# Kernel optimization log

Hardware: AMD Instinct MI355X
Metric: run time of the kernel (lower is better)

The kernel has to match this reference:

```python
import jax, jax.numpy as jnp
import numpy as np

B, S, D_IN, D_H = 2048, 256, 128, 256
C2 = 2.7193  # time-decay log offset from the original module


def setup_inputs() -> dict:
    key = jax.random.key(0)
    k0, k1, k2, k3 = jax.random.split(key, 4)
    inputs = jax.random.normal(k0, (B, S, D_IN), dtype=jnp.float32)
    # time must be increasing so intervals are positive (log(dt + 2.7193) valid)
    dt = jax.random.uniform(k1, (B, S), minval=0.1, maxval=5.0, dtype=jnp.float32)
    time = jnp.cumsum(dt, axis=1)
    Wi = jax.random.normal(k2, (D_IN, D_H), dtype=jnp.float32) / np.sqrt(D_IN).astype(np.float32)
    bi = jnp.zeros((D_H,), dtype=jnp.float32)
    Wh = jax.random.normal(k3, (D_H, D_H), dtype=jnp.float32) / np.sqrt(D_H).astype(np.float32)
    bh = jnp.zeros((D_H,), dtype=jnp.float32)
    return {"inputs": inputs, "time": time, "Wi": Wi, "bi": bi, "Wh": Wh, "bh": bh}


def reference(inputs, time, Wi, bi, Wh, bh):
    Bsz, Slen, _ = inputs.shape
    H = Wh.shape[0]
    # time points -> intervals, then decay weight 1/log(dt + c2)
    dt = time[:, 1:] - time[:, :-1]                     # [B, S-1]
    w = 1.0 / jnp.log(dt + C2)                          # [B, S-1]
    # precompute all input projections once (original recomputes per gate)
    x_proj = jnp.einsum('bsd,dh->bsh', inputs[:, :-1], Wi) + bi  # [B, S-1, H]

    def step(carry, xs):
        h, c, o = carry
        xz, wt = xs                                     # xz:[B,H], wt:[B]
        z = xz + h @ Wh + bh                            # shared gate pre-activation
        g = jax.nn.sigmoid(z)                           # f_t == i_t == o_t (same linears in source)
        C_bar = jnp.tanh(z)
        C_S = jnp.tanh(c @ Wh + bh)                     # short-term memory
        C_star = (c - C_S) + C_S * wt[:, None]          # long-term + discounted short-term
        c_new = g * C_star + g * C_bar
        h_new = g * jnp.tanh(C_bar)
        return (h_new, c_new, g), None

    zeros = jnp.zeros((Bsz, H), dtype=inputs.dtype)
    (h, c, o), _ = jax.lax.scan(
        step, (zeros, zeros, zeros),
        (jnp.swapaxes(x_proj, 0, 1), w.T),
    )
    res = o @ Wh + bh                                   # linear_hidden(o_t) of last step
    return jnp.stack((res, h, c))                       # [3, B, H]
```

## Files before the change

### kernel.cpp

```cpp
#include <hip/hip_runtime.h>

typedef __attribute__((ext_vector_type(8))) short short8;
typedef __attribute__((ext_vector_type(4))) float floatx4;
typedef __attribute__((ext_vector_type(2))) float floatx2;
typedef __attribute__((ext_vector_type(2))) unsigned uintx2;

#define LOG2E 1.44269504088896340736f

#define BAR() asm volatile("s_waitcnt lgkmcnt(0)\n\ts_barrier" ::: "memory")

__device__ __forceinline__ floatx2 F2(float v) { return (floatx2){v, v}; }

__device__ __forceinline__ unsigned short f2bf(float f) {
  unsigned u = __float_as_uint(f);
  u += 0x7FFFu + ((u >> 16) & 1u);
  return (unsigned short)(u >> 16);
}

__device__ __forceinline__ unsigned cvtpk(float lo, float hi) {
  unsigned r;
  asm("v_cvt_pk_bf16_f32 %0, %1, %2" : "=v"(r) : "v"(lo), "v"(hi));
  return r;
}

__global__ __launch_bounds__(512, 1) void tlstm_kernel(
    const float* __restrict__ x, const float* __restrict__ tim,
    const float* __restrict__ Wi, const float* __restrict__ bi,
    const float* __restrict__ Wh, const float* __restrict__ bh,
    float* __restrict__ out)
{
  __shared__ __align__(16) unsigned short Sst[2 * 4224];
  __shared__ __align__(16) unsigned short Sx[2 * 2176];
  __shared__ __align__(16) float WMt[2048];

  const int tid = threadIdx.x;
  const int wv  = tid >> 6;
  const int l   = tid & 63;
  const int q   = l >> 4;
  const int r   = l & 15;
  const int b0  = blockIdx.x * 8;

  const int col1 = wv * 32 + r;
  const int col2 = col1 + 16;

  short8 wh[2][8];
#pragma unroll
  for (int tx = 0; tx < 2; ++tx)
#pragma unroll
    for (int c = 0; c < 8; ++c)
#pragma unroll
      for (int j = 0; j < 8; ++j)
        wh[tx][c][j] = (short)f2bf(Wh[(c * 32 + q * 8 + j) * 256 + wv * 32 + tx * 16 + r]);
  short8 wi[2][4];
#pragma unroll
  for (int tx = 0; tx < 2; ++tx)
#pragma unroll
    for (int c = 0; c < 4; ++c)
#pragma unroll
      for (int j = 0; j < 8; ++j)
        wi[tx][c][j] = (short)f2bf(Wi[(c * 32 + q * 8 + j) * 256 + wv * 32 + tx * 16 + r]);
  const float bh1 = bh[col1], bh2 = bh[col2];
  const float bi1 = bi[col1], bi2 = bi[col2];

  const int raS = r * 264 + q * 8;
  const int raX = r * 136 + q * 8;
  const int wrA = (4 * q) * 264 + col1;
  const int xw  = (2 * wv + (l >> 5)) * 136 + 4 * (l & 31);
  const float* xbase = x + (long)(b0 + wv) * 32768 + (l >> 5) * 128 + 4 * (l & 31);

  {
    unsigned* S32 = (unsigned*)Sst;
    for (int i = tid; i < 2112; i += 512) S32[i] = 0;
  }
  for (int i = tid; i < 2040; i += 512) {
    int t = i >> 3, bl = i & 7;
    float t0 = tim[(b0 + bl) * 256 + t];
    float t1 = tim[(b0 + bl) * 256 + t + 1];
    WMt[i] = 1.f - 1.f / logf(t1 - t0 + 2.7193f);
  }
  {
    floatx4 v = *(const floatx4*)xbase;
    uintx2 pk = {cvtpk(v.x, v.y), cvtpk(v.z, v.w)};
    *(uintx2*)&Sx[xw] = pk;
  }
  __syncthreads();

  floatx2 cP0 = F2(0.f), cP1 = F2(0.f);
  floatx2 hP0 = F2(0.f), hP1 = F2(0.f);
  floatx2 gP0 = F2(0.f), gP1 = F2(0.f);
  int xro = 0;

  auto proc2 = [&](floatx2 zin, floatx2 cpin, floatx2& cio, floatx2& gio,
                   floatx2& hio, float wmv, int ih0, int ih1, int woff) {
    floatx2 z  = __builtin_elementwise_min(__builtin_elementwise_max(zin,  F2(-10.f)), F2(10.f));
    floatx2 cp = __builtin_elementwise_min(__builtin_elementwise_max(cpin, F2(-10.f)), F2(10.f));
    floatx2 mz = z * F2(-LOG2E);
    floatx2 u  = {__builtin_amdgcn_exp2f(mz.x), __builtin_amdgcn_exp2f(mz.y)};
    floatx2 u2 = u * u;
    floatx2 mc = cp * F2(-2.f * LOG2E);
    floatx2 v  = {__builtin_amdgcn_exp2f(mc.x), __builtin_amdgcn_exp2f(mc.y)};
    floatx2 a1 = u + F2(1.f), a2 = u2 + F2(1.f), a3 = v + F2(1.f);
    floatx2 p12 = a1 * a2;
    floatx2 pr  = p12 * a3;
    floatx2 D   = {__builtin_amdgcn_rcpf(pr.x), __builtin_amdgcn_rcpf(pr.y)};
    floatx2 Da3 = D * a3;
    floatx2 g   = Da3 * a2;
    floatx2 ir2 = Da3 * a1;
    floatx2 ir3 = D * p12;
    floatx2 Cb  = ir2 - u2 * ir2;
    floatx2 Cs  = ir3 - v * ir3;
    floatx2 Cst = cio - Cs * F2(wmv);
    floatx2 cn  = g * (Cst + Cb);
    floatx2 s   = Cb * Cb;
    floatx2 P   = F2(0.003592028f);
    P = P * s + F2(-0.008863236f);
    P = P * s + F2(0.021869488f);
    P = P * s + F2(-0.053968254f);
    P = P * s + F2(0.133333333f);
    P = P * s + F2(-0.333333333f);
    P = P * s + F2(1.0f);
    floatx2 hn = g * (Cb * P);
    unsigned pk0 = cvtpk(hn.x, cn.x);
    unsigned pk1 = cvtpk(hn.y, cn.y);
    Sst[woff + ih0]       = (unsigned short)pk0;
    Sst[woff + ih0 + 264] = (unsigned short)(pk0 >> 16);
    Sst[woff + ih1]       = (unsigned short)pk1;
    Sst[woff + ih1 + 264] = (unsigned short)(pk1 >> 16);
    cio = cn; gio = g; hio = hn;
  };

  floatx4 xa1, xa2;
  auto loadx = [&]() {
    short8 xf[4];
#pragma unroll
    for (int c = 0; c < 4; ++c)
      xf[c] = *(const short8*)&Sx[xro + raX + 32 * c];
    floatx4 x1 = {bi1, bi1, bi1, bi1};
    floatx4 x2 = {bi2, bi2, bi2, bi2};
#pragma unroll
    for (int c = 0; c < 4; ++c) {
      x1 = __builtin_amdgcn_mfma_f32_16x16x32_bf16(xf[c], wi[0][c], x1, 0, 0, 0);
      x2 = __builtin_amdgcn_mfma_f32_16x16x32_bf16(xf[c], wi[1][c], x2, 0, 0, 0);
    }
    xa1 = x1; xa2 = x2;
  };

  auto dostep = [&](int roff, int woff, int par, int wmoff) {
    short8 sf[8];
#pragma unroll
    for (int c = 0; c < 8; ++c)
      sf[c] = *(const short8*)&Sst[roff + raS + 32 * c];
    floatx4 a1e = {bh1, bh1, bh1, bh1}, a1o = {0.f, 0.f, 0.f, 0.f};
    floatx4 a2e = {bh2, bh2, bh2, bh2}, a2o = {0.f, 0.f, 0.f, 0.f};
#pragma unroll
    for (int c = 0; c < 8; c += 2) {
      a1e = __builtin_amdgcn_mfma_f32_16x16x32_bf16(sf[c],     wh[0][c],     a1e, 0, 0, 0);
      a1o = __builtin_amdgcn_mfma_f32_16x16x32_bf16(sf[c + 1], wh[0][c + 1], a1o, 0, 0, 0);
      a2e = __builtin_amdgcn_mfma_f32_16x16x32_bf16(sf[c],     wh[1][c],     a2e, 0, 0, 0);
      a2o = __builtin_amdgcn_mfma_f32_16x16x32_bf16(sf[c + 1], wh[1][c + 1], a2o, 0, 0, 0);
    }
    floatx4 A1 = a1e + a1o;
    floatx4 A2 = a2e + a2o;
    floatx2 wm = *(const floatx2*)&WMt[wmoff];
    floatx2 z0  = {A1[0] + xa1[par],     A2[0] + xa2[par]};
    floatx2 cp0 = {A1[1],                A2[1]};
    floatx2 z1  = {A1[2] + xa1[2 + par], A2[2] + xa2[2 + par]};
    floatx2 cp1 = {A1[3],                A2[3]};
    proc2(z0, cp0, cP0, gP0, hP0, wm.x, wrA,       wrA + 16,  woff);
    proc2(z1, cp1, cP1, gP1, hP1, wm.y, wrA + 528, wrA + 544, woff);
    BAR();
  };

  for (int p = 0; p < 127; ++p) {
    floatx4 nv = *(const floatx4*)(xbase + (p + 1) * 256);
    loadx();
    dostep(0, 4224, 0, 16 * p + 2 * q);
    {
      uintx2 pk = {cvtpk(nv.x, nv.y), cvtpk(nv.z, nv.w)};
      *(uintx2*)&Sx[(xro ^ 2176) + xw] = pk;
    }
    dostep(4224, 0, 1, 16 * p + 8 + 2 * q);
    xro ^= 2176;
  }

  loadx();
  dostep(0, 4224, 0, 16 * 127 + 2 * q);

  Sst[wrA]       = f2bf(gP0.x);  Sst[wrA + 264] = 0;
  Sst[wrA + 528] = f2bf(gP1.x);  Sst[wrA + 792] = 0;
  Sst[wrA + 16]  = f2bf(gP0.y);  Sst[wrA + 280] = 0;
  Sst[wrA + 544] = f2bf(gP1.y);  Sst[wrA + 808] = 0;
  BAR();
  short8 gf[8];
#pragma unroll
  for (int c = 0; c < 8; ++c)
    gf[c] = *(const short8*)&Sst[raS + 32 * c];
  floatx4 r1 = {bh1, bh1, bh1, bh1};
  floatx4 r2 = {bh2, bh2, bh2, bh2};
#pragma unroll
  for (int c = 0; c < 8; ++c) {
    r1 = __builtin_amdgcn_mfma_f32_16x16x32_bf16(gf[c], wh[0][c], r1, 0, 0, 0);
    r2 = __builtin_amdgcn_mfma_f32_16x16x32_bf16(gf[c], wh[1][c], r2, 0, 0, 0);
  }

  const long P  = 2048L * 256;
  const long o0 = (long)(b0 + 2 * q) * 256;
  const long o1 = (long)(b0 + 2 * q + 1) * 256;
  out[o0 + col1]         = r1[0];
  out[o1 + col1]         = r1[2];
  out[o0 + col2]         = r2[0];
  out[o1 + col2]         = r2[2];
  out[P + o0 + col1]     = hP0.x;
  out[P + o1 + col1]     = hP1.x;
  out[P + o0 + col2]     = hP0.y;
  out[P + o1 + col2]     = hP1.y;
  out[2 * P + o0 + col1] = cP0.x;
  out[2 * P + o1 + col1] = cP1.x;
  out[2 * P + o0 + col2] = cP0.y;
  out[2 * P + o1 + col2] = cP1.y;
}

extern "C" void kernel_launch(void* const* d_in, const int* in_sizes, int n_in,
                              void* d_out, int out_size, void* d_ws, size_t ws_size,
                              hipStream_t stream) {
  const float* xin = (const float*)d_in[0];
  const float* tim = (const float*)d_in[1];
  const float* Wi  = (const float*)d_in[2];
  const float* bi  = (const float*)d_in[3];
  const float* Wh  = (const float*)d_in[4];
  const float* bh  = (const float*)d_in[5];
  tlstm_kernel<<<dim3(256), dim3(512), 0, stream>>>(xin, tim, Wi, bi, Wh, bh, (float*)d_out);
}
```

Baseline: 254.3 us.

## Halve batch rows per block and launch twice as many blocks

Each block now handles 4 batch rows instead of 8, giving 512 blocks and allowing 2 blocks per CU via launch bounds. Each thread keeps one column pair of state instead of two, which cuts the elementwise gate work per step and halves the shared-memory footprint. The aim is to spread the serial recurrence over all CUs and overlap two blocks' latency chains per CU. In exchange, the MFMA tiles are half-filled (rows 8-15 read duplicated data), so matrix work per useful row doubles, and register pressure must fit in the 2-block limit.

Measured after the change: 347.6 us. +36.7%, slower.

```diff
diff --git a/kernel.cpp b/kernel.cpp
--- a/kernel.cpp
+++ b/kernel.cpp
@@ -3,7 +3,6 @@
 typedef __attribute__((ext_vector_type(8))) short short8;
 typedef __attribute__((ext_vector_type(4))) float floatx4;
 typedef __attribute__((ext_vector_type(2))) float floatx2;
-typedef __attribute__((ext_vector_type(2))) unsigned uintx2;
 
 #define LOG2E 1.44269504088896340736f
 
@@ -23,25 +22,29 @@
   return r;
 }
 
-__global__ __launch_bounds__(512, 1) void tlstm_kernel(
+__global__ __launch_bounds__(512, 2) void tlstm_kernel(
     const float* __restrict__ x, const float* __restrict__ tim,
     const float* __restrict__ Wi, const float* __restrict__ bi,
     const float* __restrict__ Wh, const float* __restrict__ bh,
     float* __restrict__ out)
 {
-  __shared__ __align__(16) unsigned short Sst[2 * 4224];
-  __shared__ __align__(16) unsigned short Sx[2 * 2176];
-  __shared__ __align__(16) float WMt[2048];
+  __shared__ __align__(16) unsigned short Sst[2 * 2112];
+  __shared__ __align__(16) unsigned short Sx[2 * 1088];
+  __shared__ __align__(16) float WMt[1020];
 
   const int tid = threadIdx.x;
   const int wv  = tid >> 6;
   const int l   = tid & 63;
   const int q   = l >> 4;
   const int r   = l & 15;
-  const int b0  = blockIdx.x * 8;
+  const int r8  = r & 7;
+  const int q1  = q & 1;
+  const int qt  = q >> 1;
+  const int b0  = blockIdx.x * 4;
 
   const int col1 = wv * 32 + r;
   const int col2 = col1 + 16;
+  const int wcol = wv * 32 + qt * 16 + r;
 
   short8 wh[2][8];
 #pragma unroll
@@ -62,36 +65,32 @@
   const float bh1 = bh[col1], bh2 = bh[col2];
   const float bi1 = bi[col1], bi2 = bi[col2];
 
-  const int raS = r * 264 + q * 8;
-  const int raX = r * 136 + q * 8;
-  const int wrA = (4 * q) * 264 + col1;
-  const int xw  = (2 * wv + (l >> 5)) * 136 + 4 * (l & 31);
-  const float* xbase = x + (long)(b0 + wv) * 32768 + (l >> 5) * 128 + 4 * (l & 31);
+  const int raS = r8 * 264 + q * 8;
+  const int raX = r8 * 136 + q * 8;
+  const int ih0 = (4 * q1) * 264 + wcol;
+  const int xw  = wv * 136 + 2 * l;
+  const float* xbase = x + (long)(b0 + (wv >> 1)) * 32768 + (wv & 1) * 128 + 2 * l;
 
   {
     unsigned* S32 = (unsigned*)Sst;
-    for (int i = tid; i < 2112; i += 512) S32[i] = 0;
-  }
-  for (int i = tid; i < 2040; i += 512) {
-    int t = i >> 3, bl = i & 7;
+    for (int i = tid; i < 1056; i += 512) S32[i] = 0;
+  }
+  for (int i = tid; i < 1020; i += 512) {
+    int t = i >> 2, bl = i & 3;
     float t0 = tim[(b0 + bl) * 256 + t];
     float t1 = tim[(b0 + bl) * 256 + t + 1];
     WMt[i] = 1.f - 1.f / logf(t1 - t0 + 2.7193f);
   }
   {
-    floatx4 v = *(const floatx4*)xbase;
-    uintx2 pk = {cvtpk(v.x, v.y), cvtpk(v.z, v.w)};
-    *(uintx2*)&Sx[xw] = pk;
+    floatx2 v = *(const floatx2*)xbase;
+    *(unsigned*)&Sx[xw] = cvtpk(v.x, v.y);
   }
   __syncthreads();
 
-  floatx2 cP0 = F2(0.f), cP1 = F2(0.f);
-  floatx2 hP0 = F2(0.f), hP1 = F2(0.f);
-  floatx2 gP0 = F2(0.f), gP1 = F2(0.f);
+  floatx2 cS = F2(0.f), hS = F2(0.f), gS = F2(0.f);
   int xro = 0;
 
-  auto proc2 = [&](floatx2 zin, floatx2 cpin, floatx2& cio, floatx2& gio,
-                   floatx2& hio, float wmv, int ih0, int ih1, int woff) {
+  auto proc2 = [&](floatx2 zin, floatx2 cpin, floatx2 wmv, int woff) {
     floatx2 z  = __builtin_elementwise_min(__builtin_elementwise_max(zin,  F2(-10.f)), F2(10.f));
     floatx2 cp = __builtin_elementwise_min(__builtin_elementwise_max(cpin, F2(-10.f)), F2(10.f));
     floatx2 mz = z * F2(-LOG2E);
@@ -109,7 +108,7 @@
     floatx2 ir3 = D * p12;
     floatx2 Cb  = ir2 - u2 * ir2;
     floatx2 Cs  = ir3 - v * ir3;
-    floatx2 Cst = cio - Cs * F2(wmv);
+    floatx2 Cst = cS - Cs * wmv;
     floatx2 cn  = g * (Cst + Cb);
     floatx2 s   = Cb * Cb;
     floatx2 P   = F2(0.003592028f);
@@ -124,12 +123,12 @@
     unsigned pk1 = cvtpk(hn.y, cn.y);
     Sst[woff + ih0]       = (unsigned short)pk0;
     Sst[woff + ih0 + 264] = (unsigned short)(pk0 >> 16);
-    Sst[woff + ih1]       = (unsigned short)pk1;
-    Sst[woff + ih1 + 264] = (unsigned short)(pk1 >> 16);
-    cio = cn; gio = g; hio = hn;
+    Sst[woff + ih0 + 528] = (unsigned short)pk1;
+    Sst[woff + ih0 + 792] = (unsigned short)(pk1 >> 16);
+    cS = cn; gS = g; hS = hn;
   };
 
-  floatx4 xa1, xa2;
+  floatx4 xs;
   auto loadx = [&]() {
     short8 xf[4];
 #pragma unroll
@@ -142,7 +141,7 @@
       x1 = __builtin_amdgcn_mfma_f32_16x16x32_bf16(xf[c], wi[0][c], x1, 0, 0, 0);
       x2 = __builtin_amdgcn_mfma_f32_16x16x32_bf16(xf[c], wi[1][c], x2, 0, 0, 0);
     }
-    xa1 = x1; xa2 = x2;
+    xs = qt ? x2 : x1;
   };
 
   auto dostep = [&](int roff, int woff, int par, int wmoff) {
@@ -150,46 +149,35 @@
 #pragma unroll
     for (int c = 0; c < 8; ++c)
       sf[c] = *(const short8*)&Sst[roff + raS + 32 * c];
-    floatx4 a1e = {bh1, bh1, bh1, bh1}, a1o = {0.f, 0.f, 0.f, 0.f};
-    floatx4 a2e = {bh2, bh2, bh2, bh2}, a2o = {0.f, 0.f, 0.f, 0.f};
-#pragma unroll
-    for (int c = 0; c < 8; c += 2) {
-      a1e = __builtin_amdgcn_mfma_f32_16x16x32_bf16(sf[c],     wh[0][c],     a1e, 0, 0, 0);
-      a1o = __builtin_amdgcn_mfma_f32_16x16x32_bf16(sf[c + 1], wh[0][c + 1], a1o, 0, 0, 0);
-      a2e = __builtin_amdgcn_mfma_f32_16x16x32_bf16(sf[c],     wh[1][c],     a2e, 0, 0, 0);
-      a2o = __builtin_amdgcn_mfma_f32_16x16x32_bf16(sf[c + 1], wh[1][c + 1], a2o, 0, 0, 0);
+    floatx4 a1 = {bh1, bh1, bh1, bh1};
+    floatx4 a2 = {bh2, bh2, bh2, bh2};
+#pragma unroll
+    for (int c = 0; c < 8; ++c) {
+      a1 = __builtin_amdgcn_mfma_f32_16x16x32_bf16(sf[c], wh[0][c], a1, 0, 0, 0);
+      a2 = __builtin_amdgcn_mfma_f32_16x16x32_bf16(sf[c], wh[1][c], a2, 0, 0, 0);
     }
-    floatx4 A1 = a1e + a1o;
-    floatx4 A2 = a2e + a2o;
-    floatx2 wm = *(const floatx2*)&WMt[wmoff];
-    floatx2 z0  = {A1[0] + xa1[par],     A2[0] + xa2[par]};
-    floatx2 cp0 = {A1[1],                A2[1]};
-    floatx2 z1  = {A1[2] + xa1[2 + par], A2[2] + xa2[2 + par]};
-    floatx2 cp1 = {A1[3],                A2[3]};
-    proc2(z0, cp0, cP0, gP0, hP0, wm.x, wrA,       wrA + 16,  woff);
-    proc2(z1, cp1, cP1, gP1, hP1, wm.y, wrA + 528, wrA + 544, woff);
+    floatx4 As = qt ? a2 : a1;
+    floatx2 wm = *(const floatx2*)&WMt[wmoff + 2 * q1];
+    floatx2 z  = {As[0] + xs[par], As[2] + xs[2 + par]};
+    floatx2 cp = {As[1],           As[3]};
+    proc2(z, cp, wm, woff);
     BAR();
   };
 
   for (int p = 0; p < 127; ++p) {
-    floatx4 nv = *(const floatx4*)(xbase + (p + 1) * 256);
+    floatx2 nv = *(const floatx2*)(xbase + (p + 1) * 256);
     loadx();
-    dostep(0, 4224, 0, 16 * p + 2 * q);
-    {
-      uintx2 pk = {cvtpk(nv.x, nv.y), cvtpk(nv.z, nv.w)};
-      *(uintx2*)&Sx[(xro ^ 2176) + xw] = pk;
-    }
-    dostep(4224, 0, 1, 16 * p + 8 + 2 * q);
-    xro ^= 2176;
+    dostep(0, 2112, 0, 8 * p);
+    *(unsigned*)&Sx[(xro ^ 1088) + xw] = cvtpk(nv.x, nv.y);
+    dostep(2112, 0, 1, 8 * p + 4);
+    xro ^= 1088;
   }
 
   loadx();
-  dostep(0, 4224, 0, 16 * 127 + 2 * q);
-
-  Sst[wrA]       = f2bf(gP0.x);  Sst[wrA + 264] = 0;
-  Sst[wrA + 528] = f2bf(gP1.x);  Sst[wrA + 792] = 0;
-  Sst[wrA + 16]  = f2bf(gP0.y);  Sst[wrA + 280] = 0;
-  Sst[wrA + 544] = f2bf(gP1.y);  Sst[wrA + 808] = 0;
+  dostep(0, 2112, 0, 8 * 127);
+
+  Sst[ih0]       = f2bf(gS.x);  Sst[ih0 + 264] = 0;
+  Sst[ih0 + 528] = f2bf(gS.y);  Sst[ih0 + 792] = 0;
   BAR();
   short8 gf[8];
 #pragma unroll
@@ -202,22 +190,17 @@
     r1 = __builtin_amdgcn_mfma_f32_16x16x32_bf16(gf[c], wh[0][c], r1, 0, 0, 0);
     r2 = __builtin_amdgcn_mfma_f32_16x16x32_bf16(gf[c], wh[1][c], r2, 0, 0, 0);
   }
+  floatx4 rs = qt ? r2 : r1;
 
   const long P  = 2048L * 256;
-  const long o0 = (long)(b0 + 2 * q) * 256;
-  const long o1 = (long)(b0 + 2 * q + 1) * 256;
-  out[o0 + col1]         = r1[0];
-  out[o1 + col1]         = r1[2];
-  out[o0 + col2]         = r2[0];
-  out[o1 + col2]         = r2[2];
-  out[P + o0 + col1]     = hP0.x;
-  out[P + o1 + col1]     = hP1.x;
-  out[P + o0 + col2]     = hP0.y;
-  out[P + o1 + col2]     = hP1.y;
-  out[2 * P + o0 + col1] = cP0.x;
-  out[2 * P + o1 + col1] = cP1.x;
-  out[2 * P + o0 + col2] = cP0.y;
-  out[2 * P + o1 + col2] = cP1.y;
+  const long o0 = (long)(b0 + 2 * q1) * 256;
+  const long o1 = o0 + 256;
+  out[o0 + wcol]         = rs[0];
+  out[o1 + wcol]         = rs[2];
+  out[P + o0 + wcol]     = hS.x;
+  out[P + o1 + wcol]     = hS.y;
+  out[2 * P + o0 + wcol] = cS.x;
+  out[2 * P + o1 + wcol] = cS.y;
 }
 
 extern "C" void kernel_launch(void* const* d_in, const int* in_sizes, int n_in,
@@ -229,5 +212,5 @@
   const float* bi  = (const float*)d_in[3];
   const float* Wh  = (const float*)d_in[4];
   const float* bh  = (const float*)d_in[5];
-  tlstm_kernel<<<dim3(256), dim3(512), 0, stream>>>(xin, tim, Wi, bi, Wh, bh, (float*)d_out);
-}
+  tlstm_kernel<<<dim3(512), dim3(512), 0, stream>>>(xin, tim, Wi, bi, Wh, bh, (float*)d_out);
+}
```

## Fold -log2e into weights and prefetch x projection one step ahead

Applied to the files above, without the earlier changes.

Scales Wh, Wi and both biases by -log2(e) at load time so the exp2 arguments come straight from the MFMA accumulators, which removes per-element multiplies. The final linear output is rescaled by -ln2 to undo this. The input projection for the next step pair is now computed one step early, and global x loads are prefetched two steps ahead with the first two slices staged up front, so the x MFMAs sit off the serial recurrence path. The split even/odd accumulators are replaced by single serial MFMA chains, and the lane-to-row mapping in proc2 is rearranged. Risks include extra bf16 rounding error from the scaled weights, higher register pressure, and longer MFMA dependency chains.

Measured after the change: 270.2 us. 6.2% more time.

```diff
diff --git a/kernel.cpp b/kernel.cpp
--- a/kernel.cpp
+++ b/kernel.cpp
@@ -5,7 +5,9 @@
 typedef __attribute__((ext_vector_type(2))) float floatx2;
 typedef __attribute__((ext_vector_type(2))) unsigned uintx2;
 
-#define LOG2E 1.44269504088896340736f
+#define NLOG2E -1.44269504088896340736f
+#define NLN2   -0.69314718055994530942f
+#define CLMP    14.4269504089f
 
 #define BAR() asm volatile("s_waitcnt lgkmcnt(0)\n\ts_barrier" ::: "memory")
 
@@ -50,7 +52,7 @@
     for (int c = 0; c < 8; ++c)
 #pragma unroll
       for (int j = 0; j < 8; ++j)
-        wh[tx][c][j] = (short)f2bf(Wh[(c * 32 + q * 8 + j) * 256 + wv * 32 + tx * 16 + r]);
+        wh[tx][c][j] = (short)f2bf(NLOG2E * Wh[(c * 32 + q * 8 + j) * 256 + wv * 32 + tx * 16 + r]);
   short8 wi[2][4];
 #pragma unroll
   for (int tx = 0; tx < 2; ++tx)
@@ -58,14 +60,14 @@
     for (int c = 0; c < 4; ++c)
 #pragma unroll
       for (int j = 0; j < 8; ++j)
-        wi[tx][c][j] = (short)f2bf(Wi[(c * 32 + q * 8 + j) * 256 + wv * 32 + tx * 16 + r]);
-  const float bh1 = bh[col1], bh2 = bh[col2];
-  const float bi1 = bi[col1], bi2 = bi[col2];
-
-  const int raS = r * 264 + q * 8;
-  const int raX = r * 136 + q * 8;
-  const int wrA = (4 * q) * 264 + col1;
-  const int xw  = (2 * wv + (l >> 5)) * 136 + 4 * (l & 31);
+        wi[tx][c][j] = (short)f2bf(NLOG2E * Wi[(c * 32 + q * 8 + j) * 256 + wv * 32 + tx * 16 + r]);
+  const float bh1 = NLOG2E * bh[col1], bh2 = NLOG2E * bh[col2];
+  const float bi1 = NLOG2E * bi[col1], bi2 = NLOG2E * bi[col2];
+
+  const int raS  = r * 264 + q * 8;
+  const int raX  = r * 136 + q * 8;
+  const int ihT1 = (4 * q) * 264 + col1;
+  const int xw   = (2 * wv + (l >> 5)) * 136 + 4 * (l & 31);
   const float* xbase = x + (long)(b0 + wv) * 32768 + (l >> 5) * 128 + 4 * (l & 31);
 
   {
@@ -79,26 +81,28 @@
     WMt[i] = 1.f - 1.f / logf(t1 - t0 + 2.7193f);
   }
   {
-    floatx4 v = *(const floatx4*)xbase;
-    uintx2 pk = {cvtpk(v.x, v.y), cvtpk(v.z, v.w)};
-    *(uintx2*)&Sx[xw] = pk;
+    floatx4 v0 = *(const floatx4*)xbase;
+    uintx2 p0 = {cvtpk(v0.x, v0.y), cvtpk(v0.z, v0.w)};
+    *(uintx2*)&Sx[xw] = p0;
+    floatx4 v1 = *(const floatx4*)(xbase + 256);
+    uintx2 p1 = {cvtpk(v1.x, v1.y), cvtpk(v1.z, v1.w)};
+    *(uintx2*)&Sx[2176 + xw] = p1;
   }
   __syncthreads();
 
-  floatx2 cP0 = F2(0.f), cP1 = F2(0.f);
-  floatx2 hP0 = F2(0.f), hP1 = F2(0.f);
-  floatx2 gP0 = F2(0.f), gP1 = F2(0.f);
+  floatx2 cT1 = F2(0.f), cT2 = F2(0.f);
+  floatx2 hT1 = F2(0.f), hT2 = F2(0.f);
+  floatx2 gT1 = F2(0.f), gT2 = F2(0.f);
   int xro = 0;
 
   auto proc2 = [&](floatx2 zin, floatx2 cpin, floatx2& cio, floatx2& gio,
-                   floatx2& hio, float wmv, int ih0, int ih1, int woff) {
-    floatx2 z  = __builtin_elementwise_min(__builtin_elementwise_max(zin,  F2(-10.f)), F2(10.f));
-    floatx2 cp = __builtin_elementwise_min(__builtin_elementwise_max(cpin, F2(-10.f)), F2(10.f));
-    floatx2 mz = z * F2(-LOG2E);
-    floatx2 u  = {__builtin_amdgcn_exp2f(mz.x), __builtin_amdgcn_exp2f(mz.y)};
+                   floatx2& hio, floatx2 wm, int ih, int woff) {
+    floatx2 z  = __builtin_elementwise_min(__builtin_elementwise_max(zin,  F2(-CLMP)), F2(CLMP));
+    floatx2 cp = __builtin_elementwise_min(__builtin_elementwise_max(cpin, F2(-CLMP)), F2(CLMP));
+    floatx2 u  = {__builtin_amdgcn_exp2f(z.x), __builtin_amdgcn_exp2f(z.y)};
     floatx2 u2 = u * u;
-    floatx2 mc = cp * F2(-2.f * LOG2E);
-    floatx2 v  = {__builtin_amdgcn_exp2f(mc.x), __builtin_amdgcn_exp2f(mc.y)};
+    floatx2 c2 = cp + cp;
+    floatx2 v  = {__builtin_amdgcn_exp2f(c2.x), __builtin_amdgcn_exp2f(c2.y)};
     floatx2 a1 = u + F2(1.f), a2 = u2 + F2(1.f), a3 = v + F2(1.f);
     floatx2 p12 = a1 * a2;
     floatx2 pr  = p12 * a3;
@@ -109,7 +113,7 @@
     floatx2 ir3 = D * p12;
     floatx2 Cb  = ir2 - u2 * ir2;
     floatx2 Cs  = ir3 - v * ir3;
-    floatx2 Cst = cio - Cs * F2(wmv);
+    floatx2 Cst = cio - Cs * wm;
     floatx2 cn  = g * (Cst + Cb);
     floatx2 s   = Cb * Cb;
     floatx2 P   = F2(0.003592028f);
@@ -122,19 +126,18 @@
     floatx2 hn = g * (Cb * P);
     unsigned pk0 = cvtpk(hn.x, cn.x);
     unsigned pk1 = cvtpk(hn.y, cn.y);
-    Sst[woff + ih0]       = (unsigned short)pk0;
-    Sst[woff + ih0 + 264] = (unsigned short)(pk0 >> 16);
-    Sst[woff + ih1]       = (unsigned short)pk1;
-    Sst[woff + ih1 + 264] = (unsigned short)(pk1 >> 16);
+    Sst[woff + ih]       = (unsigned short)pk0;
+    Sst[woff + ih + 264] = (unsigned short)(pk0 >> 16);
+    Sst[woff + ih + 528] = (unsigned short)pk1;
+    Sst[woff + ih + 792] = (unsigned short)(pk1 >> 16);
     cio = cn; gio = g; hio = hn;
   };
 
-  floatx4 xa1, xa2;
-  auto loadx = [&]() {
+  auto loadx = [&](int xoff, floatx4& x1o, floatx4& x2o) {
     short8 xf[4];
 #pragma unroll
     for (int c = 0; c < 4; ++c)
-      xf[c] = *(const short8*)&Sx[xro + raX + 32 * c];
+      xf[c] = *(const short8*)&Sx[xoff + raX + 32 * c];
     floatx4 x1 = {bi1, bi1, bi1, bi1};
     floatx4 x2 = {bi2, bi2, bi2, bi2};
 #pragma unroll
@@ -142,54 +145,54 @@
       x1 = __builtin_amdgcn_mfma_f32_16x16x32_bf16(xf[c], wi[0][c], x1, 0, 0, 0);
       x2 = __builtin_amdgcn_mfma_f32_16x16x32_bf16(xf[c], wi[1][c], x2, 0, 0, 0);
     }
-    xa1 = x1; xa2 = x2;
+    x1o = x1; x2o = x2;
   };
 
-  auto dostep = [&](int roff, int woff, int par, int wmoff) {
+  auto dostep = [&](int roff, int woff, floatx4 xa1, floatx4 xa2, int par, int wmoff) {
     short8 sf[8];
 #pragma unroll
     for (int c = 0; c < 8; ++c)
       sf[c] = *(const short8*)&Sst[roff + raS + 32 * c];
-    floatx4 a1e = {bh1, bh1, bh1, bh1}, a1o = {0.f, 0.f, 0.f, 0.f};
-    floatx4 a2e = {bh2, bh2, bh2, bh2}, a2o = {0.f, 0.f, 0.f, 0.f};
-#pragma unroll
-    for (int c = 0; c < 8; c += 2) {
-      a1e = __builtin_amdgcn_mfma_f32_16x16x32_bf16(sf[c],     wh[0][c],     a1e, 0, 0, 0);
-      a1o = __builtin_amdgcn_mfma_f32_16x16x32_bf16(sf[c + 1], wh[0][c + 1], a1o, 0, 0, 0);
-      a2e = __builtin_amdgcn_mfma_f32_16x16x32_bf16(sf[c],     wh[1][c],     a2e, 0, 0, 0);
-      a2o = __builtin_amdgcn_mfma_f32_16x16x32_bf16(sf[c + 1], wh[1][c + 1], a2o, 0, 0, 0);
-    }
-    floatx4 A1 = a1e + a1o;
-    floatx4 A2 = a2e + a2o;
+    floatx4 a1 = {bh1, bh1, bh1, bh1};
+#pragma unroll
+    for (int c = 0; c < 8; ++c)
+      a1 = __builtin_amdgcn_mfma_f32_16x16x32_bf16(sf[c], wh[0][c], a1, 0, 0, 0);
+    floatx4 a2 = {bh2, bh2, bh2, bh2};
+#pragma unroll
+    for (int c = 0; c < 8; ++c)
+      a2 = __builtin_amdgcn_mfma_f32_16x16x32_bf16(sf[c], wh[1][c], a2, 0, 0, 0);
     floatx2 wm = *(const floatx2*)&WMt[wmoff];
-    floatx2 z0  = {A1[0] + xa1[par],     A2[0] + xa2[par]};
-    floatx2 cp0 = {A1[1],                A2[1]};
-    floatx2 z1  = {A1[2] + xa1[2 + par], A2[2] + xa2[2 + par]};
-    floatx2 cp1 = {A1[3],                A2[3]};
-    proc2(z0, cp0, cP0, gP0, hP0, wm.x, wrA,       wrA + 16,  woff);
-    proc2(z1, cp1, cP1, gP1, hP1, wm.y, wrA + 528, wrA + 544, woff);
+    proc2((floatx2){a1[0] + xa1[par], a1[2] + xa1[2 + par]},
+          (floatx2){a1[1], a1[3]}, cT1, gT1, hT1, wm, ihT1, woff);
+    proc2((floatx2){a2[0] + xa2[par], a2[2] + xa2[2 + par]},
+          (floatx2){a2[1], a2[3]}, cT2, gT2, hT2, wm, ihT1 + 16, woff);
     BAR();
   };
 
+  floatx4 xc1, xc2;
+  loadx(0, xc1, xc2);
+
   for (int p = 0; p < 127; ++p) {
-    floatx4 nv = *(const floatx4*)(xbase + (p + 1) * 256);
-    loadx();
-    dostep(0, 4224, 0, 16 * p + 2 * q);
+    const int pn = (p < 125) ? p + 2 : 127;
+    floatx4 nv = *(const floatx4*)(xbase + (long)pn * 256);
+    dostep(0, 4224, xc1, xc2, 0, 16 * p + 2 * q);
     {
       uintx2 pk = {cvtpk(nv.x, nv.y), cvtpk(nv.z, nv.w)};
-      *(uintx2*)&Sx[(xro ^ 2176) + xw] = pk;
+      *(uintx2*)&Sx[xro + xw] = pk;
     }
-    dostep(4224, 0, 1, 16 * p + 8 + 2 * q);
+    floatx4 xn1, xn2;
+    loadx(xro ^ 2176, xn1, xn2);
+    dostep(4224, 0, xc1, xc2, 1, 16 * p + 8 + 2 * q);
+    xc1 = xn1; xc2 = xn2;
     xro ^= 2176;
   }
 
-  loadx();
-  dostep(0, 4224, 0, 16 * 127 + 2 * q);
-
-  Sst[wrA]       = f2bf(gP0.x);  Sst[wrA + 264] = 0;
-  Sst[wrA + 528] = f2bf(gP1.x);  Sst[wrA + 792] = 0;
-  Sst[wrA + 16]  = f2bf(gP0.y);  Sst[wrA + 280] = 0;
-  Sst[wrA + 544] = f2bf(gP1.y);  Sst[wrA + 808] = 0;
+  dostep(0, 4224, xc1, xc2, 0, 16 * 127 + 2 * q);
+
+  Sst[ihT1]       = f2bf(gT1.x);  Sst[ihT1 + 264] = 0;
+  Sst[ihT1 + 528] = f2bf(gT1.y);  Sst[ihT1 + 792] = 0;
+  Sst[ihT1 + 16]  = f2bf(gT2.x);  Sst[ihT1 + 280] = 0;
+  Sst[ihT1 + 544] = f2bf(gT2.y);  Sst[ihT1 + 808] = 0;
   BAR();
   short8 gf[8];
 #pragma unroll
@@ -205,19 +208,19 @@
 
   const long P  = 2048L * 256;
   const long o0 = (long)(b0 + 2 * q) * 256;
-  const long o1 = (long)(b0 + 2 * q + 1) * 256;
-  out[o0 + col1]         = r1[0];
-  out[o1 + col1]         = r1[2];
-  out[o0 + col2]         = r2[0];
-  out[o1 + col2]         = r2[2];
-  out[P + o0 + col1]     = hP0.x;
-  out[P + o1 + col1]     = hP1.x;
-  out[P + o0 + col2]     = hP0.y;
-  out[P + o1 + col2]     = hP1.y;
-  out[2 * P + o0 + col1] = cP0.x;
-  out[2 * P + o1 + col1] = cP1.x;
-  out[2 * P + o0 + col2] = cP0.y;
-  out[2 * P + o1 + col2] = cP1.y;
+  const long o1 = o0 + 256;
+  out[o0 + col1]         = NLN2 * r1[0];
+  out[o1 + col1]         = NLN2 * r1[2];
+  out[o0 + col2]         = NLN2 * r2[0];
+  out[o1 + col2]         = NLN2 * r2[2];
+  out[P + o0 + col1]     = hT1.x;
+  out[P + o1 + col1]     = hT1.y;
+  out[P + o0 + col2]     = hT2.x;
+  out[P + o1 + col2]     = hT2.y;
+  out[2 * P + o0 + col1] = cT1.x;
+  out[2 * P + o1 + col1] = cT1.y;
+  out[2 * P + o0 + col2] = cT2.x;
+  out[2 * P + o1 + col2] = cT2.y;
 }
 
 extern "C" void kernel_launch(void* const* d_in, const int* in_sizes, int n_in,
```
